# Kernel optimization log

Hardware: AMD Instinct MI355X
Metric: run time of the kernel (lower is better)

Reference implementation:

```python
import jax, jax.numpy as jnp
import numpy as np

B, S, H, I, E, K = 4, 2048, 2048, 5632, 8, 2


def setup_inputs() -> dict:
    key = jax.random.key(0)
    k0, k1, k2, k3, k4 = jax.random.split(key, 5)
    std_p = 1.0 / np.sqrt(H)
    return {
        "hidden_states": jax.random.normal(k0, (B, S, H), dtype=jnp.float32),
        "router_w": jax.random.normal(k1, (E, H), dtype=jnp.float32) * 0.02,
        "w_gate": jax.random.normal(k2, (E, H, I), dtype=jnp.float32) * std_p,
        "w_up": jax.random.normal(k3, (E, H, I), dtype=jnp.float32) * std_p,
        "w_down": jax.random.normal(k4, (E, I, H), dtype=jnp.float32) * (1.0 / np.sqrt(I)),
    }


def reference(hidden_states, router_w, w_gate, w_up, w_down):
    b, s, h = hidden_states.shape
    x = hidden_states.reshape(-1, h)                       # [T, H]
    router_logits = x @ router_w.T                          # [T, E]
    routing_weights = jax.nn.softmax(router_logits, axis=-1)
    top_w, top_i = jax.lax.top_k(routing_weights, K)        # [T, K]
    top_w = top_w / jnp.sum(top_w, axis=-1, keepdims=True)  # renormalize over top-k
    # combine[t, e] = sum_k top_w[t, k] * (top_i[t, k] == e)
    combine = jnp.sum(jax.nn.one_hot(top_i, E, dtype=top_w.dtype) * top_w[..., None], axis=1)  # [T, E]
    out = jnp.zeros_like(x)
    for e in range(E):  # small fixed expert count
        # SwiGLU expert MLP: down(silu(gate(x)) * up(x))
        act = jax.nn.silu(x @ w_gate[e]) * (x @ w_up[e])    # [T, I]
        out = out + (act @ w_down[e]) * combine[:, e:e + 1]
    return (out.reshape(b, s, h),
            router_logits.reshape(b, s, E),
            top_i.reshape(b, s, K),
            top_w.reshape(b, s, K))
```

## Files before the change

kernel.cpp:

```cpp
#include <hip/hip_runtime.h>
#include <hip/hip_bf16.h>
#include <stdint.h>

#define NTOK 8192
#define HD   2048
#define ID   5632
#define NE   8
#define NASSIGN (NTOK * 2)
#define MAXT256 (NASSIGN / 256 + NE)

typedef __attribute__((ext_vector_type(8))) short  bf16x8;
typedef __attribute__((ext_vector_type(4))) float  f32x4;
typedef __attribute__((ext_vector_type(8))) unsigned short u16x8;

__device__ __forceinline__ unsigned short f2bf(float f) {
  union { float f; unsigned int u; } c; c.f = f;
  unsigned int lsb = (c.u >> 16) & 1u;
  return (unsigned short)((c.u + 0x7fffu + lsb) >> 16);
}

__device__ __forceinline__ void async16(const void* g, void* l) {
  __builtin_amdgcn_global_load_lds(
      (const __attribute__((address_space(1))) void*)g,
      (__attribute__((address_space(3))) void*)l, 16, 0, 0);
}

__global__ __launch_bounds__(256) void k_router(
    const float* __restrict__ x, const float* __restrict__ rw,
    float* __restrict__ out_logits, float* __restrict__ out_topi,
    float* __restrict__ out_topw,
    int* __restrict__ tk_e, float* __restrict__ tk_w, int* __restrict__ cnts)
{
  const int wid = threadIdx.x >> 6, lane = threadIdx.x & 63;
  const int t = blockIdx.x * 4 + wid;
  const float* xr = x + (size_t)t * HD;
  float acc[NE];
#pragma unroll
  for (int e = 0; e < NE; e++) acc[e] = 0.f;
#pragma unroll
  for (int i = 0; i < 8; i++) {
    const int col = lane * 4 + i * 256;
    const float4 xv = *(const float4*)(xr + col);
#pragma unroll
    for (int e = 0; e < NE; e++) {
      const float4 wv = *(const float4*)(rw + e * HD + col);
      acc[e] += xv.x * wv.x + xv.y * wv.y + xv.z * wv.z + xv.w * wv.w;
    }
  }
#pragma unroll
  for (int e = 0; e < NE; e++)
    for (int o = 32; o >= 1; o >>= 1) acc[e] += __shfl_xor(acc[e], o, 64);

  if (lane == 0) {
    int i1 = 0;
#pragma unroll
    for (int e = 1; e < NE; e++) if (acc[e] > acc[i1]) i1 = e;
    int i2 = (i1 == 0) ? 1 : 0;
#pragma unroll
    for (int e = 0; e < NE; e++) if (e != i1 && acc[e] > acc[i2]) i2 = e;
    float p2 = __expf(acc[i2] - acc[i1]);
    float s  = 1.f + p2;
    float w1 = 1.f / s, w2 = p2 / s;
#pragma unroll
    for (int e = 0; e < NE; e++) out_logits[(size_t)t * NE + e] = acc[e];
    out_topi[t * 2 + 0] = (float)i1; out_topi[t * 2 + 1] = (float)i2;
    out_topw[t * 2 + 0] = w1;        out_topw[t * 2 + 1] = w2;
    tk_e[t * 2 + 0] = i1; tk_e[t * 2 + 1] = i2;
    tk_w[t * 2 + 0] = w1; tk_w[t * 2 + 1] = w2;
    atomicAdd(&cnts[i1], 1); atomicAdd(&cnts[i2], 1);
  }
}

__global__ void k_scan(const int* __restrict__ cnts, int* __restrict__ offs,
                       int* __restrict__ cursor, int* __restrict__ tile_e,
                       int* __restrict__ tile_rt, int* __restrict__ ntiles) {
  if (threadIdx.x == 0) {
    int s = 0, nt = 0;
    for (int e = 0; e < NE; e++) {
      offs[e] = s; cursor[e] = s;
      int ntl = (cnts[e] + 255) >> 8;
      for (int i = 0; i < ntl; i++) { tile_e[nt] = e; tile_rt[nt] = i; nt++; }
      s += cnts[e];
    }
    ntiles[0] = nt;
  }
}

__global__ void k_assign(const int* __restrict__ tk_e, const float* __restrict__ tk_w,
                         int* __restrict__ cursor, int* __restrict__ perm,
                         float* __restrict__ pw, int* __restrict__ inv) {
  int t = blockIdx.x * 256 + threadIdx.x;
  if (t >= NTOK) return;
#pragma unroll
  for (int k = 0; k < 2; k++) {
    int e = tk_e[t * 2 + k];
    int pos = atomicAdd(&cursor[e], 1);
    perm[pos] = t;
    pw[pos] = tk_w[t * 2 + k];
    inv[t * 2 + k] = pos;
  }
}

__global__ __launch_bounds__(256) void k_gather(const float* __restrict__ x,
    const int* __restrict__ perm, unsigned short* __restrict__ xg) {
  const int r = blockIdx.x;
  const int tok = perm[r];
  const float* src = x + (size_t)tok * HD;
  unsigned short* dst = xg + (size_t)r * HD;
  const int c = threadIdx.x * 8;
  float4 a = *(const float4*)(src + c);
  float4 b = *(const float4*)(src + c + 4);
  u16x8 o;
  o[0] = f2bf(a.x); o[1] = f2bf(a.y); o[2] = f2bf(a.z); o[3] = f2bf(a.w);
  o[4] = f2bf(b.x); o[5] = f2bf(b.y); o[6] = f2bf(b.z); o[7] = f2bf(b.w);
  *(u16x8*)(dst + c) = o;
}

__global__ __launch_bounds__(256) void k_conv64(const float* __restrict__ in0,
    const float* __restrict__ in1, unsigned short* __restrict__ out0,
    unsigned short* __restrict__ out1, int R, int C, int nmat) {
  __shared__ unsigned short tlb[64][72];
  const int z = blockIdx.z;
  const int mat = (nmat == 2) ? (z & 1) : 0;
  const int e   = (nmat == 2) ? (z >> 1) : z;
  const float* in = ((mat == 0) ? in0 : in1) + (size_t)e * R * C;
  unsigned short* out = ((mat == 0) ? out0 : out1) + (size_t)e * (size_t)R * C;
  const int tid = threadIdx.x;
  const int c0 = blockIdx.x * 64, r0 = blockIdx.y * 64;
#pragma unroll
  for (int pass = 0; pass < 4; ++pass) {
    const int kr = pass * 16 + (tid >> 4);
    const int cc = (tid & 15) * 4;
    const float4 v = *(const float4*)(in + (size_t)(r0 + kr) * C + c0 + cc);
    tlb[cc + 0][kr] = f2bf(v.x); tlb[cc + 1][kr] = f2bf(v.y);
    tlb[cc + 2][kr] = f2bf(v.z); tlb[cc + 3][kr] = f2bf(v.w);
  }
  __syncthreads();
#pragma unroll
  for (int pass = 0; pass < 2; ++pass) {
    const int n = pass * 32 + (tid >> 3);
    const int k = (tid & 7) * 8;
    *(u16x8*)(out + (size_t)(c0 + n) * R + r0 + k) = *(const u16x8*)&tlb[n][k];
  }
}

#define HBF(b,kh) (((b)*2+(kh))*32768)

__global__ __launch_bounds__(512, 2) void k_gemm_gu256f(
    const unsigned short* __restrict__ A,
    const unsigned short* __restrict__ BgT, const unsigned short* __restrict__ BuT,
    const int* __restrict__ cnts, const int* __restrict__ offs,
    const int* __restrict__ tile_e, const int* __restrict__ tile_rt,
    const int* __restrict__ ntiles, unsigned short* __restrict__ gact)
{
  const int raw = blockIdx.x;
  const int v = (raw & 7) * ((int)gridDim.x >> 3) + (raw >> 3);
  const int ct = v / MAXT256;
  const int ti = v % MAXT256;
  if (ti >= ntiles[0]) return;
  const int e = tile_e[ti], rt = tile_rt[ti];
  const int cnt = cnts[e], off = offs[e];
  const int tid = threadIdx.x;

  __shared__ __align__(16) char smem[131072];

  const unsigned short* Bg = BgT + (size_t)e * (size_t)ID * HD;
  const unsigned short* Bu = BuT + (size_t)e * (size_t)ID * HD;
  const size_t arow0 = (size_t)off + (size_t)rt * 256;
  const size_t bcol0 = (size_t)ct * 128;

  const int r0s = tid >> 2;
  const int c0s = (((tid & 3) ^ ((tid >> 3) & 3)) * 8);

  const int NT = HD / 64, NIT = NT / 2;

  auto STAGE_A = [&](int bb, int kh, int kt) {
    const int kc = kt * 64 + kh * 32;
    async16(A + (arow0 + r0s) * (size_t)HD + kc + c0s, smem + HBF(bb,kh) + tid * 16);
    async16(A + (arow0 + 128 + r0s) * (size_t)HD + kc + c0s, smem + HBF(bb,kh) + 8192 + tid * 16);
  };
  auto STAGE_B = [&](int bb, int kh, int kt) {
    const int kc = kt * 64 + kh * 32;
    async16(Bg + (bcol0 + r0s) * (size_t)HD + kc + c0s, smem + HBF(bb,kh) + 16384 + tid * 16);
    async16(Bu + (bcol0 + r0s) * (size_t)HD + kc + c0s, smem + HBF(bb,kh) + 24576 + tid * 16);
  };

  f32x4 accg[8][2], accu[8][2];
#pragma unroll
  for (int m = 0; m < 8; m++)
#pragma unroll
    for (int n = 0; n < 2; n++) { accg[m][n] = (f32x4)0.f; accu[m][n] = (f32x4)0.f; }

  const int lane = tid & 63, wid = tid >> 6;
  const int wm = wid >> 2, wn = wid & 3;
  const int fr = lane & 15;
  const int slot = ((lane >> 4) ^ ((fr >> 1) & 3));
  const int laddr = (fr << 6) + (slot << 4);

  STAGE_A(0,0,0); STAGE_B(0,0,0); STAGE_A(0,1,0); STAGE_B(0,1,0);
  STAGE_A(1,0,1); STAGE_B(1,0,1);
  asm volatile("s_waitcnt vmcnt(4)" ::: "memory");
  asm volatile("s_barrier" ::: "memory");

  constexpr int SB[8]  = {1,1,0,0,0,0,1,1};
  constexpr int SOP[8] = {0,1,0,1,0,1,0,1};
  constexpr int SKH[8] = {1,1,0,0,1,1,0,0};
  constexpr int SKO[8] = {1,1,2,2,2,2,3,3};

  bf16x8 bgr[2], bur[2];
  for (int i = 0; i < NIT; ++i) {
#pragma unroll
    for (int p = 0; p < 8; ++p) {
      const int b = p >> 2, kh = (p >> 1) & 1, mh = p & 1;
      bf16x8 afr[4];
#pragma unroll
      for (int t = 0; t < 4; t++)
        afr[t] = *(const bf16x8*)(smem + HBF(b,kh) + ((wm*128 + mh*64 + t*16) << 6) + laddr);
      if (mh == 0) {
#pragma unroll
        for (int t = 0; t < 2; t++) {
          bgr[t] = *(const bf16x8*)(smem + HBF(b,kh) + 16384 + ((wn*32 + t*16) << 6) + laddr);
          bur[t] = *(const bf16x8*)(smem + HBF(b,kh) + 24576 + ((wn*32 + t*16) << 6) + laddr);
        }
      }
      {
        int kt = 2 * i + SKO[p]; kt = kt < NT - 1 ? kt : NT - 1;
        if (SOP[p] == 0) STAGE_A(SB[p], SKH[p], kt);
        else             STAGE_B(SB[p], SKH[p], kt);
      }
      asm volatile("s_barrier" ::: "memory");
      __builtin_amdgcn_s_setprio(1);
#pragma unroll
      for (int t = 0; t < 4; t++)
#pragma unroll
        for (int n = 0; n < 2; n++) {
          accg[mh*4 + t][n] = __builtin_amdgcn_mfma_f32_16x16x32_bf16(afr[t], bgr[n], accg[mh*4 + t][n], 0, 0, 0);
          accu[mh*4 + t][n] = __builtin_amdgcn_mfma_f32_16x16x32_bf16(afr[t], bur[n], accu[mh*4 + t][n], 0, 0, 0);
        }
      __builtin_amdgcn_s_setprio(0);
      if (p == 3 || p == 7) asm volatile("s_waitcnt vmcnt(4)" ::: "memory");
      asm volatile("s_barrier" ::: "memory");
    }
  }
  asm volatile("s_waitcnt vmcnt(0)" ::: "memory");

  const int crow = (lane >> 4) * 4, ccol = lane & 15;
  const int rbase = rt * 256 + wm * 128;
#pragma unroll
  for (int mt = 0; mt < 8; ++mt) {
#pragma unroll
    for (int j = 0; j < 4; ++j) {
      const int rl = rbase + mt * 16 + crow + j;
      if (rl >= cnt) continue;
      const size_t grow = (size_t)off + rl;
#pragma unroll
      for (int nt = 0; nt < 2; ++nt) {
        const int col = (int)bcol0 + wn * 32 + nt * 16 + ccol;
        const float g = accg[mt][nt][j], u = accu[mt][nt][j];
        const float a = g / (1.f + __expf(-g)) * u;
        gact[grow * (size_t)ID + col] = f2bf(a);
      }
    }
  }
}

#define HB(b,kh,op) (((((b)*2+(kh))*2)+(op))*16384)

__global__ __launch_bounds__(512, 2) void k_gemm_dn256(
    const unsigned short* __restrict__ A,
    const unsigned short* __restrict__ Wbase,
    const int* __restrict__ cnts, const int* __restrict__ offs,
    const int* __restrict__ tile_e, const int* __restrict__ tile_rt,
    const int* __restrict__ ntiles,
    const float* __restrict__ pw, float* __restrict__ dbuf)
{
  const int raw = blockIdx.x;
  const int v = (raw & 7) * ((int)gridDim.x >> 3) + (raw >> 3);
  const int ti = v % MAXT256;
  const int rest = v / MAXT256;
  const int ksplit = rest & 1;
  const int ct = rest >> 1;
  if (ti >= ntiles[0]) return;
  const int e = tile_e[ti], rt = tile_rt[ti];
  const int cnt = cnts[e], off = offs[e];
  const int tid = threadIdx.x;

  __shared__ __align__(16) char smem[131072];

  const unsigned short* W = Wbase + (size_t)e * (size_t)HD * ID;
  const size_t arow0 = (size_t)off + (size_t)rt * 256;
  const size_t bcol0 = (size_t)ct * 256;
  const int kbase = ksplit * (ID / 2);

  const int r0s = tid >> 2;
  const int c0s = (((tid & 3) ^ ((tid >> 3) & 3)) * 8);

  const int NT = (ID / 2) / 64, NIT = NT / 2;

  auto STAGE_A = [&](int bb, int kh, int kt) {
    const int kc = kbase + kt * 64 + kh * 32;
    async16(A + (arow0 + r0s) * (size_t)ID + kc + c0s, smem + HB(bb,kh,0) + tid * 16);
    async16(A + (arow0 + 128 + r0s) * (size_t)ID + kc + c0s, smem + HB(bb,kh,0) + 8192 + tid * 16);
  };
  auto STAGE_B = [&](int bb, int kh, int kt) {
    const int kc = kbase + kt * 64 + kh * 32;
    async16(W + (bcol0 + r0s) * (size_t)ID + kc + c0s, smem + HB(bb,kh,1) + tid * 16);
    async16(W + (bcol0 + 128 + r0s) * (size_t)ID + kc + c0s, smem + HB(bb,kh,1) + 8192 + tid * 16);
  };

  f32x4 acc[8][4];
#pragma unroll
  for (int m = 0; m < 8; m++)
#pragma unroll
    for (int n = 0; n < 4; n++) acc[m][n] = (f32x4)0.f;

  const int lane = tid & 63, wid = tid >> 6;
  const int wm = wid >> 2, wn = wid & 3;
  const int fr = lane & 15;
  const int slot = ((lane >> 4) ^ ((fr >> 1) & 3));
  const int laddr = (fr << 6) + (slot << 4);

  STAGE_A(0,0,0); STAGE_B(0,0,0); STAGE_A(0,1,0); STAGE_B(0,1,0);
  STAGE_A(1,0,1); STAGE_B(1,0,1);
  asm volatile("s_waitcnt vmcnt(4)" ::: "memory");
  asm volatile("s_barrier" ::: "memory");

  constexpr int SB[8]  = {1,1,0,0,0,0,1,1};
  constexpr int SOP[8] = {0,1,0,1,0,1,0,1};
  constexpr int SKH[8] = {1,1,0,0,1,1,0,0};
  constexpr int SKO[8] = {1,1,2,2,2,2,3,3};

  bf16x8 bfr[4];
  for (int i = 0; i < NIT; ++i) {
#pragma unroll
    for (int p = 0; p < 8; ++p) {
      const int b = p >> 2, kh = (p >> 1) & 1, mh = p & 1;
      bf16x8 afr[4];
#pragma unroll
      for (int t = 0; t < 4; t++)
        afr[t] = *(const bf16x8*)(smem + HB(b,kh,0) + ((wm*128 + mh*64 + t*16) << 6) + laddr);
      if (mh == 0) {
#pragma unroll
        for (int t = 0; t < 4; t++)
          bfr[t] = *(const bf16x8*)(smem + HB(b,kh,1) + ((wn*64 + t*16) << 6) + laddr);
      }
      {
        int kt = 2 * i + SKO[p]; kt = kt < NT - 1 ? kt : NT - 1;
        if (SOP[p] == 0) STAGE_A(SB[p], SKH[p], kt);
        else             STAGE_B(SB[p], SKH[p], kt);
      }
      asm volatile("s_barrier" ::: "memory");
      __builtin_amdgcn_s_setprio(1);
#pragma unroll
      for (int t = 0; t < 4; t++)
#pragma unroll
        for (int n = 0; n < 4; n++)
          acc[mh*4 + t][n] = __builtin_amdgcn_mfma_f32_16x16x32_bf16(afr[t], bfr[n], acc[mh*4 + t][n], 0, 0, 0);
      __builtin_amdgcn_s_setprio(0);
      if (p == 3 || p == 7) asm volatile("s_waitcnt vmcnt(4)" ::: "memory");
      asm volatile("s_barrier" ::: "memory");
    }
  }
  asm volatile("s_waitcnt vmcnt(0)" ::: "memory");

  float* db = dbuf + (size_t)ksplit * (size_t)NASSIGN * HD;
  const int crow = (lane >> 4) * 4, ccol = lane & 15;
  const int rbase = rt * 256 + wm * 128;
#pragma unroll
  for (int mt = 0; mt < 8; ++mt) {
#pragma unroll
    for (int j = 0; j < 4; ++j) {
      const int rl = rbase + mt * 16 + crow + j;
      if (rl >= cnt) continue;
      const size_t grow = (size_t)off + rl;
      const float wgt = pw[grow];
#pragma unroll
      for (int nt = 0; nt < 4; ++nt) {
        const int col = (int)bcol0 + wn * 64 + nt * 16 + ccol;
        db[grow * (size_t)HD + col] = acc[mt][nt][j] * wgt;
      }
    }
  }
}

__global__ __launch_bounds__(256) void k_combine(const float* __restrict__ dbuf,
    const int* __restrict__ inv, float* __restrict__ out) {
  const int t = blockIdx.x;
  const int p0 = inv[t * 2], p1 = inv[t * 2 + 1];
  const float* d1 = dbuf + (size_t)NASSIGN * HD;
  const float4* a0 = (const float4*)(dbuf + (size_t)p0 * HD);
  const float4* a1 = (const float4*)(dbuf + (size_t)p1 * HD);
  const float4* b0 = (const float4*)(d1 + (size_t)p0 * HD);
  const float4* b1 = (const float4*)(d1 + (size_t)p1 * HD);
  float4* o = (float4*)(out + (size_t)t * HD);
#pragma unroll
  for (int i = 0; i < 2; i++) {
    int c = threadIdx.x + i * 256;
    float4 x0 = a0[c], x1 = a1[c], y0 = b0[c], y1 = b1[c];
    o[c] = make_float4(x0.x + x1.x + y0.x + y1.x, x0.y + x1.y + y0.y + y1.y,
                       x0.z + x1.z + y0.z + y1.z, x0.w + x1.w + y0.w + y1.w);
  }
}

extern "C" void kernel_launch(void* const* d_in, const int* in_sizes, int n_in,
                              void* d_out, int out_size, void* d_ws, size_t ws_size,
                              hipStream_t stream) {
  const float* x  = (const float*)d_in[0];
  const float* rw = (const float*)d_in[1];
  const float* wg = (const float*)d_in[2];
  const float* wu = (const float*)d_in[3];
  const float* wd = (const float*)d_in[4];

  float* outp       = (float*)d_out;
  float* out_logits = outp + (size_t)NTOK * HD;
  float* out_topi   = out_logits + (size_t)NTOK * NE;
  float* out_topw   = out_topi + (size_t)NTOK * 2;

  char* w = (char*)d_ws;
  int*   cnts    = (int*)(w + 0);
  int*   offs    = (int*)(w + 64);
  int*   cursor  = (int*)(w + 128);
  int*   ntiles  = (int*)(w + 192);
  int*   tile_e  = (int*)(w + 256);
  int*   tile_rt = (int*)(w + 1280);
  int*   tk_e    = (int*)(w + 4096);
  float* tk_w    = (float*)(w + 4096 + 65536);
  int*   perm    = (int*)(w + 4096 + 2 * 65536);
  float* pw      = (float*)(w + 4096 + 3 * 65536);
  int*   inv     = (int*)(w + 4096 + 4 * 65536);

  char* big = w + (1 << 20);
  unsigned short* xg = (unsigned short*)big;
  const size_t XG_E = (size_t)(NASSIGN + 256) * HD;
  unsigned short* wgT = xg + XG_E;
  const size_t WT_E = (size_t)NE * ID * HD;
  unsigned short* wuT  = wgT + WT_E;
  unsigned short* wdT  = wuT + WT_E;
  unsigned short* gact = wdT + WT_E;
  const size_t GA_E = (size_t)(NASSIGN + 256) * ID;
  float* dbuf = (float*)(gact + GA_E);

  hipMemsetAsync(d_ws, 0, 256, stream);

  k_conv64<<<dim3(ID / 64, HD / 64, 2 * NE), 256, 0, stream>>>(
      wg, wu, wgT, wuT, HD, ID, 2);
  k_conv64<<<dim3(HD / 64, ID / 64, NE), 256, 0, stream>>>(
      wd, nullptr, wdT, nullptr, ID, HD, 1);

  k_router<<<NTOK / 4, 256, 0, stream>>>(x, rw, out_logits, out_topi, out_topw,
                                         tk_e, tk_w, cnts);
  k_scan<<<1, 64, 0, stream>>>(cnts, offs, cursor, tile_e, tile_rt, ntiles);
  k_assign<<<NTOK / 256, 256, 0, stream>>>(tk_e, tk_w, cursor, perm, pw, inv);
  k_gather<<<NASSIGN, 256, 0, stream>>>(x, perm, xg);

  k_gemm_gu256f<<<dim3((ID / 128) * MAXT256), 512, 0, stream>>>(
      xg, wgT, wuT, cnts, offs, tile_e, tile_rt, ntiles, gact);
  k_gemm_dn256<<<dim3((HD / 256) * 2 * MAXT256), 512, 0, stream>>>(
      gact, wdT, cnts, offs, tile_e, tile_rt, ntiles, pw, dbuf);
  k_combine<<<NTOK, 256, 0, stream>>>(dbuf, inv, outp);
}
```

Measured before the change: 1.849 ms.

## Replace 8-phase double-buffer schedule with 4-stage 32-wide K ring buffer

Both grouped GEMMs (gate/up and down) now stream K in 32-wide slices through a four-slot shared-memory ring, prefetching three slices ahead. Each slice is split into two M-halves with one barrier each, instead of the old 8-phase table with two barriers per phase. The goal is fewer barriers per unit of K and a deeper load-ahead to hide global latency. The waitcnt is issued before the LDS reads with no barrier between them, so one thread may read a slot another thread's loads have not yet filled. The epilogue indexing is rewritten but maps to the same rows as before.

```diff
diff --git a/kernel.cpp b/kernel.cpp
--- a/kernel.cpp
+++ b/kernel.cpp
@@ -144,7 +144,7 @@
   }
 }
 
-#define HBF(b,kh) (((b)*2+(kh))*32768)
+#define GBUF(b) ((b) * 32768)
 
 __global__ __launch_bounds__(512, 2) void k_gemm_gu256f(
     const unsigned short* __restrict__ A,
@@ -172,17 +172,17 @@
   const int r0s = tid >> 2;
   const int c0s = (((tid & 3) ^ ((tid >> 3) & 3)) * 8);
 
-  const int NT = HD / 64, NIT = NT / 2;
-
-  auto STAGE_A = [&](int bb, int kh, int kt) {
-    const int kc = kt * 64 + kh * 32;
-    async16(A + (arow0 + r0s) * (size_t)HD + kc + c0s, smem + HBF(bb,kh) + tid * 16);
-    async16(A + (arow0 + 128 + r0s) * (size_t)HD + kc + c0s, smem + HBF(bb,kh) + 8192 + tid * 16);
+  const int NTS = HD / 32;
+
+  auto STAGE_A = [&](int bb, int kt) {
+    const int kc = kt * 32;
+    async16(A + (arow0 + r0s) * (size_t)HD + kc + c0s, smem + GBUF(bb) + tid * 16);
+    async16(A + (arow0 + 128 + r0s) * (size_t)HD + kc + c0s, smem + GBUF(bb) + 8192 + tid * 16);
   };
-  auto STAGE_B = [&](int bb, int kh, int kt) {
-    const int kc = kt * 64 + kh * 32;
-    async16(Bg + (bcol0 + r0s) * (size_t)HD + kc + c0s, smem + HBF(bb,kh) + 16384 + tid * 16);
-    async16(Bu + (bcol0 + r0s) * (size_t)HD + kc + c0s, smem + HBF(bb,kh) + 24576 + tid * 16);
+  auto STAGE_B = [&](int bb, int kt) {
+    const int kc = kt * 32;
+    async16(Bg + (bcol0 + r0s) * (size_t)HD + kc + c0s, smem + GBUF(bb) + 16384 + tid * 16);
+    async16(Bu + (bcol0 + r0s) * (size_t)HD + kc + c0s, smem + GBUF(bb) + 24576 + tid * 16);
   };
 
   f32x4 accg[8][2], accu[8][2];
@@ -197,50 +197,58 @@
   const int slot = ((lane >> 4) ^ ((fr >> 1) & 3));
   const int laddr = (fr << 6) + (slot << 4);
 
-  STAGE_A(0,0,0); STAGE_B(0,0,0); STAGE_A(0,1,0); STAGE_B(0,1,0);
-  STAGE_A(1,0,1); STAGE_B(1,0,1);
-  asm volatile("s_waitcnt vmcnt(4)" ::: "memory");
+  STAGE_A(0, 0); STAGE_B(0, 0);
+  STAGE_A(1, 1); STAGE_B(1, 1);
+  STAGE_A(2, 2); STAGE_B(2, 2);
+  asm volatile("s_waitcnt vmcnt(8)" ::: "memory");
   asm volatile("s_barrier" ::: "memory");
 
-  constexpr int SB[8]  = {1,1,0,0,0,0,1,1};
-  constexpr int SOP[8] = {0,1,0,1,0,1,0,1};
-  constexpr int SKH[8] = {1,1,0,0,1,1,0,0};
-  constexpr int SKO[8] = {1,1,2,2,2,2,3,3};
-
   bf16x8 bgr[2], bur[2];
-  for (int i = 0; i < NIT; ++i) {
-#pragma unroll
-    for (int p = 0; p < 8; ++p) {
-      const int b = p >> 2, kh = (p >> 1) & 1, mh = p & 1;
+  for (int s = 0; s < NTS; ++s) {
+    const int bi = s & 3;
+    char* base = smem + GBUF(bi);
+    int sn = s + 3; sn = sn < NTS - 1 ? sn : NTS - 1;
+    const int bn = (s + 3) & 3;
+    asm volatile("s_waitcnt vmcnt(8)" ::: "memory");
+    {
       bf16x8 afr[4];
 #pragma unroll
       for (int t = 0; t < 4; t++)
-        afr[t] = *(const bf16x8*)(smem + HBF(b,kh) + ((wm*128 + mh*64 + t*16) << 6) + laddr);
-      if (mh == 0) {
-#pragma unroll
-        for (int t = 0; t < 2; t++) {
-          bgr[t] = *(const bf16x8*)(smem + HBF(b,kh) + 16384 + ((wn*32 + t*16) << 6) + laddr);
-          bur[t] = *(const bf16x8*)(smem + HBF(b,kh) + 24576 + ((wn*32 + t*16) << 6) + laddr);
-        }
+        afr[t] = *(const bf16x8*)(base + ((wm*128 + t*16) << 6) + laddr);
+#pragma unroll
+      for (int t = 0; t < 2; t++) {
+        bgr[t] = *(const bf16x8*)(base + 16384 + ((wn*32 + t*16) << 6) + laddr);
+        bur[t] = *(const bf16x8*)(base + 24576 + ((wn*32 + t*16) << 6) + laddr);
       }
-      {
-        int kt = 2 * i + SKO[p]; kt = kt < NT - 1 ? kt : NT - 1;
-        if (SOP[p] == 0) STAGE_A(SB[p], SKH[p], kt);
-        else             STAGE_B(SB[p], SKH[p], kt);
-      }
-      asm volatile("s_barrier" ::: "memory");
+      STAGE_A(bn, sn);
       __builtin_amdgcn_s_setprio(1);
 #pragma unroll
       for (int t = 0; t < 4; t++)
 #pragma unroll
         for (int n = 0; n < 2; n++) {
-          accg[mh*4 + t][n] = __builtin_amdgcn_mfma_f32_16x16x32_bf16(afr[t], bgr[n], accg[mh*4 + t][n], 0, 0, 0);
-          accu[mh*4 + t][n] = __builtin_amdgcn_mfma_f32_16x16x32_bf16(afr[t], bur[n], accu[mh*4 + t][n], 0, 0, 0);
+          accg[t][n] = __builtin_amdgcn_mfma_f32_16x16x32_bf16(afr[t], bgr[n], accg[t][n], 0, 0, 0);
+          accu[t][n] = __builtin_amdgcn_mfma_f32_16x16x32_bf16(afr[t], bur[n], accu[t][n], 0, 0, 0);
         }
       __builtin_amdgcn_s_setprio(0);
-      if (p == 3 || p == 7) asm volatile("s_waitcnt vmcnt(4)" ::: "memory");
-      asm volatile("s_barrier" ::: "memory");
-    }
+    }
+    asm volatile("s_barrier" ::: "memory");
+    {
+      bf16x8 afr[4];
+#pragma unroll
+      for (int t = 0; t < 4; t++)
+        afr[t] = *(const bf16x8*)(base + ((wm*128 + 64 + t*16) << 6) + laddr);
+      STAGE_B(bn, sn);
+      __builtin_amdgcn_s_setprio(1);
+#pragma unroll
+      for (int t = 0; t < 4; t++)
+#pragma unroll
+        for (int n = 0; n < 2; n++) {
+          accg[4 + t][n] = __builtin_amdgcn_mfma_f32_16x16x32_bf16(afr[t], bgr[n], accg[4 + t][n], 0, 0, 0);
+          accu[4 + t][n] = __builtin_amdgcn_mfma_f32_16x16x32_bf16(afr[t], bur[n], accu[4 + t][n], 0, 0, 0);
+        }
+      __builtin_amdgcn_s_setprio(0);
+    }
+    asm volatile("s_barrier" ::: "memory");
   }
   asm volatile("s_waitcnt vmcnt(0)" ::: "memory");
 
@@ -250,21 +258,20 @@
   for (int mt = 0; mt < 8; ++mt) {
 #pragma unroll
     for (int j = 0; j < 4; ++j) {
-      const int rl = rbase + mt * 16 + crow + j;
+      const int rl = rbase + (mt & 3) * 16 + (mt >> 2) * 64 + crow + j;
       if (rl >= cnt) continue;
       const size_t grow = (size_t)off + rl;
 #pragma unroll
       for (int nt = 0; nt < 2; ++nt) {
         const int col = (int)bcol0 + wn * 32 + nt * 16 + ccol;
-        const float g = accg[mt][nt][j], u = accu[mt][nt][j];
+        const float g = accg[(mt >> 2) * 4 + (mt & 3)][nt][j];
+        const float u = accu[(mt >> 2) * 4 + (mt & 3)][nt][j];
         const float a = g / (1.f + __expf(-g)) * u;
         gact[grow * (size_t)ID + col] = f2bf(a);
       }
     }
   }
 }
-
-#define HB(b,kh,op) (((((b)*2+(kh))*2)+(op))*16384)
 
 __global__ __launch_bounds__(512, 2) void k_gemm_dn256(
     const unsigned short* __restrict__ A,
@@ -295,17 +302,17 @@
   const int r0s = tid >> 2;
   const int c0s = (((tid & 3) ^ ((tid >> 3) & 3)) * 8);
 
-  const int NT = (ID / 2) / 64, NIT = NT / 2;
-
-  auto STAGE_A = [&](int bb, int kh, int kt) {
-    const int kc = kbase + kt * 64 + kh * 32;
-    async16(A + (arow0 + r0s) * (size_t)ID + kc + c0s, smem + HB(bb,kh,0) + tid * 16);
-    async16(A + (arow0 + 128 + r0s) * (size_t)ID + kc + c0s, smem + HB(bb,kh,0) + 8192 + tid * 16);
+  const int NTS = (ID / 2) / 32;
+
+  auto STAGE_A = [&](int bb, int kt) {
+    const int kc = kbase + kt * 32;
+    async16(A + (arow0 + r0s) * (size_t)ID + kc + c0s, smem + GBUF(bb) + tid * 16);
+    async16(A + (arow0 + 128 + r0s) * (size_t)ID + kc + c0s, smem + GBUF(bb) + 8192 + tid * 16);
   };
-  auto STAGE_B = [&](int bb, int kh, int kt) {
-    const int kc = kbase + kt * 64 + kh * 32;
-    async16(W + (bcol0 + r0s) * (size_t)ID + kc + c0s, smem + HB(bb,kh,1) + tid * 16);
-    async16(W + (bcol0 + 128 + r0s) * (size_t)ID + kc + c0s, smem + HB(bb,kh,1) + 8192 + tid * 16);
+  auto STAGE_B = [&](int bb, int kt) {
+    const int kc = kbase + kt * 32;
+    async16(W + (bcol0 + r0s) * (size_t)ID + kc + c0s, smem + GBUF(bb) + 16384 + tid * 16);
+    async16(W + (bcol0 + 128 + r0s) * (size_t)ID + kc + c0s, smem + GBUF(bb) + 24576 + tid * 16);
   };
 
   f32x4 acc[8][4];
@@ -320,46 +327,52 @@
   const int slot = ((lane >> 4) ^ ((fr >> 1) & 3));
   const int laddr = (fr << 6) + (slot << 4);
 
-  STAGE_A(0,0,0); STAGE_B(0,0,0); STAGE_A(0,1,0); STAGE_B(0,1,0);
-  STAGE_A(1,0,1); STAGE_B(1,0,1);
-  asm volatile("s_waitcnt vmcnt(4)" ::: "memory");
+  STAGE_A(0, 0); STAGE_B(0, 0);
+  STAGE_A(1, 1); STAGE_B(1, 1);
+  STAGE_A(2, 2); STAGE_B(2, 2);
+  asm volatile("s_waitcnt vmcnt(8)" ::: "memory");
   asm volatile("s_barrier" ::: "memory");
 
-  constexpr int SB[8]  = {1,1,0,0,0,0,1,1};
-  constexpr int SOP[8] = {0,1,0,1,0,1,0,1};
-  constexpr int SKH[8] = {1,1,0,0,1,1,0,0};
-  constexpr int SKO[8] = {1,1,2,2,2,2,3,3};
-
   bf16x8 bfr[4];
-  for (int i = 0; i < NIT; ++i) {
-#pragma unroll
-    for (int p = 0; p < 8; ++p) {
-      const int b = p >> 2, kh = (p >> 1) & 1, mh = p & 1;
+  for (int s = 0; s < NTS; ++s) {
+    const int bi = s & 3;
+    char* base = smem + GBUF(bi);
+    int sn = s + 3; sn = sn < NTS - 1 ? sn : NTS - 1;
+    const int bn = (s + 3) & 3;
+    asm volatile("s_waitcnt vmcnt(8)" ::: "memory");
+    {
       bf16x8 afr[4];
 #pragma unroll
       for (int t = 0; t < 4; t++)
-        afr[t] = *(const bf16x8*)(smem + HB(b,kh,0) + ((wm*128 + mh*64 + t*16) << 6) + laddr);
-      if (mh == 0) {
-#pragma unroll
-        for (int t = 0; t < 4; t++)
-          bfr[t] = *(const bf16x8*)(smem + HB(b,kh,1) + ((wn*64 + t*16) << 6) + laddr);
-      }
-      {
-        int kt = 2 * i + SKO[p]; kt = kt < NT - 1 ? kt : NT - 1;
-        if (SOP[p] == 0) STAGE_A(SB[p], SKH[p], kt);
-        else             STAGE_B(SB[p], SKH[p], kt);
-      }
-      asm volatile("s_barrier" ::: "memory");
+        afr[t] = *(const bf16x8*)(base + ((wm*128 + t*16) << 6) + laddr);
+#pragma unroll
+      for (int t = 0; t < 4; t++)
+        bfr[t] = *(const bf16x8*)(base + 16384 + ((wn*64 + t*16) << 6) + laddr);
+      STAGE_A(bn, sn);
       __builtin_amdgcn_s_setprio(1);
 #pragma unroll
       for (int t = 0; t < 4; t++)
 #pragma unroll
         for (int n = 0; n < 4; n++)
-          acc[mh*4 + t][n] = __builtin_amdgcn_mfma_f32_16x16x32_bf16(afr[t], bfr[n], acc[mh*4 + t][n], 0, 0, 0);
+          acc[t][n] = __builtin_amdgcn_mfma_f32_16x16x32_bf16(afr[t], bfr[n], acc[t][n], 0, 0, 0);
       __builtin_amdgcn_s_setprio(0);
-      if (p == 3 || p == 7) asm volatile("s_waitcnt vmcnt(4)" ::: "memory");
-      asm volatile("s_barrier" ::: "memory");
-    }
+    }
+    asm volatile("s_barrier" ::: "memory");
+    {
+      bf16x8 afr[4];
+#pragma unroll
+      for (int t = 0; t < 4; t++)
+        afr[t] = *(const bf16x8*)(base + ((wm*128 + 64 + t*16) << 6) + laddr);
+      STAGE_B(bn, sn);
+      __builtin_amdgcn_s_setprio(1);
+#pragma unroll
+      for (int t = 0; t < 4; t++)
+#pragma unroll
+        for (int n = 0; n < 4; n++)
+          acc[4 + t][n] = __builtin_amdgcn_mfma_f32_16x16x32_bf16(afr[t], bfr[n], acc[4 + t][n], 0, 0, 0);
+      __builtin_amdgcn_s_setprio(0);
+    }
+    asm volatile("s_barrier" ::: "memory");
   }
   asm volatile("s_waitcnt vmcnt(0)" ::: "memory");
 
@@ -370,14 +383,14 @@
   for (int mt = 0; mt < 8; ++mt) {
 #pragma unroll
     for (int j = 0; j < 4; ++j) {
-      const int rl = rbase + mt * 16 + crow + j;
+      const int rl = rbase + (mt & 3) * 16 + (mt >> 2) * 64 + crow + j;
       if (rl >= cnt) continue;
       const size_t grow = (size_t)off + rl;
       const float wgt = pw[grow];
 #pragma unroll
       for (int nt = 0; nt < 4; ++nt) {
         const int col = (int)bcol0 + wn * 64 + nt * 16 + ccol;
-        db[grow * (size_t)HD + col] = acc[mt][nt][j] * wgt;
+        db[grow * (size_t)HD + col] = acc[(mt >> 2) * 4 + (mt & 3)][nt][j] * wgt;
       }
     }
   }
```

After: 1.813 ms. About the same (-1.9%).
